# Optimization experiments

Measured on AMD Instinct MI355X. Metric: run time of the kernel, lower is better.

The kernel has to match this reference:

```python
import jax, jax.numpy as jnp
import numpy as np

# ----- config (matches init_kwargs) -----
DATA_SIZE = 128
WIDTH = 512
DEPTH = 3          # hidden layers in eqx.nn.MLP
NUM_BLOCKS = 2
BATCH = 512
NSTEPS = 10        # (t1 - t0) / dt0 = 1.0 / 0.1
T1 = 1.0
DT = -0.1          # integrate t1 -> t0

# Tsit5 Butcher tableau (5th-order solution weights; b7 = 0 so stage 7 is skipped)
TS_C = [0.0, 0.161, 0.327, 0.9, 0.9800255409045097, 1.0]
TS_A = [
    [],
    [0.161],
    [-0.008480655492356989, 0.335480655492357],
    [2.8971530571054935, -6.359448489975075, 4.3622954328695815],
    [5.325864828439257, -11.748883564062828, 7.4955393428898365, -0.09249506636175525],
    [5.86145544294642, -12.92096931784711, 8.159367898576159, -0.071584973281401, -0.028269050394068383],
]
TS_B = [0.09646076681806523, 0.01, 0.4798896504144996, 1.379008574103742, -3.290069515436081, 2.324710524099774]


def setup_inputs() -> dict:
    key = jax.random.key(0)
    ks = jax.random.split(key, 10)
    d, w, nb = DATA_SIZE, WIDTH, NUM_BLOCKS
    in0 = d + 1  # autonomous=False: t is concatenated to y

    def init(k, shape, fan_in):
        return jax.random.normal(k, shape, dtype=jnp.float32) / np.sqrt(fan_in).astype(np.float32)

    return {
        "y": jax.random.normal(ks[0], (BATCH, d), dtype=jnp.float32),
        "Ws0": init(ks[1], (nb, in0, w), in0), "bs0": init(ks[2], (nb, w), w),
        "Ws1": init(ks[3], (nb, w, w), w),     "bs1": init(ks[4], (nb, w), w),
        "Ws2": init(ks[5], (nb, w, w), w),     "bs2": init(ks[6], (nb, w), w),
        "Ws3": init(ks[7], (nb, w, d), w),     "bs3": init(ks[8], (nb, d), d),
    }


def _mlp(inp, layers):
    # inp: [in_size] vector (per-sample), relu hidden activations, linear output
    h = inp
    for W, b in layers[:-1]:
        h = jax.nn.relu(h @ W + b)
    W, b = layers[-1]
    return h @ W + b


def _field_and_trace(t, y, layers):
    # y: [B, d]. Exact log-det trace via vmapped vjp over identity (exact_logp_wrapper).
    eye = jnp.eye(DATA_SIZE, dtype=y.dtype)

    def single(yy):
        fn = lambda z: _mlp(jnp.concatenate([jnp.full((1,), t, yy.dtype), z]), layers)
        f, vjp_fn = jax.vjp(fn, yy)
        (dfdy,) = jax.vmap(vjp_fn)(eye)  # [d, d] Jacobian
        return f, jnp.trace(dfdy)

    return jax.vmap(single)(y)


def _solve_block(y, lp, layers):
    # Fixed-step Tsit5 on augmented state (y, logp), t1 -> t0, 10 steps.
    def step(carry, n):
        y, lp = carry
        t = jnp.float32(T1) + jnp.float32(DT) * n.astype(jnp.float32)
        ky, klp = [], []
        for i in range(6):
            ti = t + jnp.float32(TS_C[i] * DT)
            yi = y
            for j in range(i):
                yi = yi + jnp.float32(DT * TS_A[i][j]) * ky[j]
            fy, flp = _field_and_trace(ti, yi, layers)
            ky.append(fy)
            klp.append(flp)
        for i in range(6):
            y = y + jnp.float32(DT * TS_B[i]) * ky[i]
            lp = lp + jnp.float32(DT * TS_B[i]) * klp[i]
        return (y, lp), None

    (y, lp), _ = jax.lax.scan(step, (y, lp), jnp.arange(NSTEPS))
    return y, lp


def reference(y, Ws0, bs0, Ws1, bs1, Ws2, bs2, Ws3, bs3):
    lp = jnp.zeros((y.shape[0],), dtype=y.dtype)  # delta log-likelihood
    for b in range(NUM_BLOCKS):
        layers = [(Ws0[b], bs0[b]), (Ws1[b], bs1[b]), (Ws2[b], bs2[b]), (Ws3[b], bs3[b])]
        y, lp = _solve_block(y, lp, layers)
    # normal_log_likelihood (faithful to source: log(2*pi) NOT scaled by d)
    log2pi = np.float32(np.log(2.0 * np.pi))
    return lp + (-0.5) * (log2pi + jnp.sum(y * y, axis=-1))
```

## Files before the change

kernel.cpp:

```cpp
#include <hip/hip_runtime.h>


using short8 = __attribute__((ext_vector_type(8))) short;
using u16x8  = __attribute__((ext_vector_type(8))) unsigned short;
using f32x4v = __attribute__((ext_vector_type(4))) float;
using i32x4  = __attribute__((ext_vector_type(4))) int;
using u32x4  = __attribute__((ext_vector_type(4))) unsigned;
using i32x16 = __attribute__((ext_vector_type(16))) int;

__device__ __forceinline__ unsigned short f2bf(float f) {
  union { float f; unsigned u; } v; v.f = f;
  unsigned r = v.u + 0x7fffu + ((v.u >> 16) & 1u);
  return (unsigned short)(r >> 16);
}
__device__ __forceinline__ float bf2f(unsigned short h) {
  union { unsigned u; float f; } v; v.u = ((unsigned)h) << 16; return v.f;
}
__device__ __forceinline__ signed char q8(float v, float inv) {
  float r = rintf(v * inv);
  r = fminf(fmaxf(r, -127.f), 127.f);
  return (signed char)(int)r;
}

typedef const __attribute__((address_space(1))) void gas_t;
typedef __attribute__((address_space(3))) void las_t;
__device__ __forceinline__ void gl_lds16(const void* g, void* l) {
  __builtin_amdgcn_global_load_lds((gas_t*)g, (las_t*)l, 16, 0, 0);
}

struct Coef6 { float v[6]; };

#define INV_S0 254.0f
#define INV_S1 508.0f
#define SCALE_J 7.7500155e-06f
#define SCALE_G 3.8750077e-06f

__global__ __launch_bounds__(256) void init_state(const float* __restrict__ y_in,
                                                  float* __restrict__ y,
                                                  float* __restrict__ lp) {
  int i = blockIdx.x * 256 + threadIdx.x;
  if (i < 512 * 128) y[i] = y_in[i];
  if (i < 512) lp[i] = 0.f;
}

__global__ __launch_bounds__(256) void cast_weights(
    const float* __restrict__ W0, const float* __restrict__ W1,
    const float* __restrict__ W2, const float* __restrict__ W3,
    signed char* __restrict__ w0q,
    unsigned short* __restrict__ w0tH, unsigned short* __restrict__ w0tL,
    unsigned short* __restrict__ w1tH, unsigned short* __restrict__ w1tL,
    signed char* __restrict__ w1q,
    unsigned short* __restrict__ w2tH, unsigned short* __restrict__ w2tL,
    unsigned short* __restrict__ w3tH, unsigned short* __restrict__ w3tL,
    signed char* __restrict__ w3q, signed char* __restrict__ w2q) {
  int i = blockIdx.x * 256 + threadIdx.x;
  if (i < 65536) {
    int j = i >> 9, a = i & 511;
    w0q[i] = q8(W0[(1 + j) * 512 + a], INV_S0);
    return;
  }
  i -= 65536;
  if (i >= 2 * 65536 + 2 * 262144) {
    int q = i - (2 * 65536 + 2 * 262144);
    if (q < 262144) w2q[q] = q8(W2[q], INV_S1);
    return;
  }
  float v;
  unsigned short* dh;
  unsigned short* dl;
  signed char* qd = nullptr;
  int di;
  if (i < 65536) {
    int n = i >> 7, k = i & 127;
    v = W0[(1 + k) * 512 + n]; dh = w0tH; dl = w0tL; di = i;
  } else if (i < 65536 + 262144) {
    int q = i - 65536; int n = q >> 9, k = q & 511;
    v = W1[k * 512 + n]; dh = w1tH; dl = w1tL; di = q; qd = w1q;
  } else if (i < 65536 + 2 * 262144) {
    int q = i - 65536 - 262144; int c = q >> 9, b = q & 511;
    v = W2[b * 512 + c]; dh = w2tH; dl = w2tL; di = q;
  } else {
    int q = i - 65536 - 2 * 262144; int j = q >> 9, c = q & 511;
    v = W3[c * 128 + j]; dh = w3tH; dl = w3tL; di = q; qd = w3q;
  }
  unsigned short hi = f2bf(v);
  dh[di] = hi;
  dl[di] = f2bf(v - bf2f(hi));
  if (qd) qd[di] = q8(v, INV_S1);
}

template <bool RELU>
__global__ __launch_bounds__(256, 2) void fwd_mfma(
    const unsigned short* __restrict__ Ahi, const unsigned short* __restrict__ Alo,
    const unsigned short* __restrict__ WtH, const unsigned short* __restrict__ WtL,
    const float* __restrict__ bias,
    float* __restrict__ Cf, unsigned short* __restrict__ Hhi,
    unsigned short* __restrict__ Hlo, int N, int K) {
  __shared__ unsigned short AsH[2][4096], AsL[2][4096], BsH[2][4096], BsL[2][4096];
  const int t = threadIdx.x, l = t & 63, w = t >> 6;
  const int wm = w >> 1, wn = w & 1, lr = l & 15, lg = l >> 4;
  const int m0 = blockIdx.y * 32, n0 = blockIdx.x * 32;
  const int lr7 = lr & 7;

  auto stage = [&](int cur, int k0) {
#pragma unroll
    for (int r = 0; r < 2; ++r) {
      int g = r * 256 + t;
      int row = g >> 4, gc = g & 15;
      size_t co = (size_t)k0 + ((gc ^ (row & 7)) << 3);
      size_t ao = (size_t)(m0 + row) * K + co;
      size_t bo = (size_t)(n0 + row) * K + co;
      int db = (r * 256 + (t & 192)) * 16;
      gl_lds16(Ahi + ao, (char*)AsH[cur] + db);
      gl_lds16(Alo + ao, (char*)AsL[cur] + db);
      gl_lds16(WtH + bo, (char*)BsH[cur] + db);
      gl_lds16(WtL + bo, (char*)BsL[cur] + db);
    }
  };

  f32x4v acc = {0.f, 0.f, 0.f, 0.f};
  stage(0, 0);
  __syncthreads();
  int cur = 0;
  for (int k0 = 0; k0 < K; k0 += 128) {
    if (k0 + 128 < K) stage(cur ^ 1, k0 + 128);
#pragma unroll
    for (int ks = 0; ks < 4; ++ks) {
      int sl = ((ks * 4 + lg) ^ lr7) << 4;
      int ab = (wm * 16 + lr) * 256 + sl;
      int bb = (wn * 16 + lr) * 256 + sl;
      short8 ah = *(const short8*)((const char*)AsH[cur] + ab);
      short8 al = *(const short8*)((const char*)AsL[cur] + ab);
      short8 bh = *(const short8*)((const char*)BsH[cur] + bb);
      short8 bl = *(const short8*)((const char*)BsL[cur] + bb);
      acc = __builtin_amdgcn_mfma_f32_16x16x32_bf16(ah, bh, acc, 0, 0, 0);
      acc = __builtin_amdgcn_mfma_f32_16x16x32_bf16(ah, bl, acc, 0, 0, 0);
      acc = __builtin_amdgcn_mfma_f32_16x16x32_bf16(al, bh, acc, 0, 0, 0);
    }
    __syncthreads();
    cur ^= 1;
  }

  int n = n0 + wn * 16 + lr;
  float be = bias[n];
#pragma unroll
  for (int r = 0; r < 4; ++r) {
    int m = m0 + wm * 16 + lg * 4 + r;
    float v = acc[r] + be;
    if (RELU) {
      v = fmaxf(v, 0.f);
      unsigned short h = f2bf(v);
      Hhi[m * N + n] = h;
      Hlo[m * N + n] = f2bf(v - bf2f(h));
    } else {
      Cf[m * N + n] = v;
    }
  }
}

__global__ __launch_bounds__(256, 2) void jac_l0(
    int l0n,
    const signed char* __restrict__ w1q, const signed char* __restrict__ w0q,
    const signed char* __restrict__ w2q, const signed char* __restrict__ w3q,
    const unsigned short* __restrict__ d0m, const unsigned short* __restrict__ d1m,
    const unsigned short* __restrict__ d2m, float* __restrict__ klp,
    const float* __restrict__ yb, const float* __restrict__ kyb, Coef6 ca, int nc,
    const unsigned short* __restrict__ WtH, const unsigned short* __restrict__ WtL,
    const float* __restrict__ bias, const float* __restrict__ wrow0, float tval,
    unsigned short* __restrict__ Hhi, unsigned short* __restrict__ Hlo) {
  __shared__ __align__(16) char smraw[68672];
  const int t = threadIdx.x, l = t & 63, w = t >> 6;

  if ((int)blockIdx.x < l0n) {
    unsigned short* AsH = (unsigned short*)(smraw);
    unsigned short* AsL = (unsigned short*)(smraw + 8192);
    unsigned short* BsH = (unsigned short*)(smraw + 16384);
    unsigned short* BsL = (unsigned short*)(smraw + 24576);
    const int lb = blockIdx.x;
    const int wm = w >> 1, wn = w & 1, lr = l & 15, lg = l >> 4, lr7 = lr & 7;
    const int m0 = (lb >> 4) * 32, n0 = (lb & 15) * 32;

#pragma unroll
    for (int r = 0; r < 2; ++r) {
      int g = r * 256 + t;
      int row = g >> 4;
      int gc = (g & 15) ^ (row & 7);
      size_t bo = (size_t)(n0 + row) * 128 + gc * 8;
      int db = (r * 256 + (t & 192)) * 16;
      gl_lds16(WtH + bo, (char*)BsH + db);
      gl_lds16(WtL + bo, (char*)BsL + db);
    }
    {
      int row = t >> 3, seg = t & 7;
      int gidx = (m0 + row) * 128 + seg * 16;
      float x[16];
#pragma unroll
      for (int q = 0; q < 4; ++q)
        *(float4*)&x[q * 4] = *(const float4*)&yb[gidx + q * 4];
      for (int j2 = 0; j2 < nc; ++j2) {
        float c = ca.v[j2];
#pragma unroll
        for (int q = 0; q < 4; ++q) {
          float4 u = *(const float4*)&kyb[j2 * 65536 + gidx + q * 4];
          x[q * 4 + 0] = fmaf(c, u.x, x[q * 4 + 0]);
          x[q * 4 + 1] = fmaf(c, u.y, x[q * 4 + 1]);
          x[q * 4 + 2] = fmaf(c, u.z, x[q * 4 + 2]);
          x[q * 4 + 3] = fmaf(c, u.w, x[q * 4 + 3]);
        }
      }
      u16x8 h8[2], l8[2];
#pragma unroll
      for (int e = 0; e < 16; ++e) {
        unsigned short hh = f2bf(x[e]);
        h8[e >> 3][e & 7] = hh;
        l8[e >> 3][e & 7] = f2bf(x[e] - bf2f(hh));
      }
#pragma unroll
      for (int h = 0; h < 2; ++h) {
        int gx = (seg * 2 + h) ^ (row & 7);
        *(u16x8*)((char*)AsH + row * 256 + gx * 16) = h8[h];
        *(u16x8*)((char*)AsL + row * 256 + gx * 16) = l8[h];
      }
    }
    __syncthreads();

    f32x4v acc = {0.f, 0.f, 0.f, 0.f};
#pragma unroll
    for (int ks = 0; ks < 4; ++ks) {
      int sl = ((ks * 4 + lg) ^ lr7) << 4;
      int ab = (wm * 16 + lr) * 256 + sl;
      int bb = (wn * 16 + lr) * 256 + sl;
      short8 ah = *(const short8*)((const char*)AsH + ab);
      short8 al = *(const short8*)((const char*)AsL + ab);
      short8 bh = *(const short8*)((const char*)BsH + bb);
      short8 bl = *(const short8*)((const char*)BsL + bb);
      acc = __builtin_amdgcn_mfma_f32_16x16x32_bf16(ah, bh, acc, 0, 0, 0);
      acc = __builtin_amdgcn_mfma_f32_16x16x32_bf16(ah, bl, acc, 0, 0, 0);
      acc = __builtin_amdgcn_mfma_f32_16x16x32_bf16(al, bh, acc, 0, 0, 0);
    }

    int n = n0 + wn * 16 + lr;
    float be = fmaf(tval, wrow0[n], bias[n]);
#pragma unroll
    for (int r = 0; r < 4; ++r) {
      int m = m0 + wm * 16 + lg * 4 + r;
      float v = fmaxf(acc[r] + be, 0.f);
      unsigned short h = f2bf(v);
      Hhi[m * 512 + n] = h;
      Hlo[m * 512 + n] = f2bf(v - bf2f(h));
    }
    return;
  }

  signed char* As = (signed char*)smraw;
  signed char* Bs = (signed char*)(smraw + 32768);
  unsigned char* Ms8 = (unsigned char*)(smraw + 65536);
  float* red = (float*)(smraw + 68608);
  const int jx = blockIdx.x - l0n;
  const int cb = jx & 3, s0 = (jx >> 2) * 2;
  const int wm = w >> 1, wn = w & 1;
  const int lr31 = l & 31, hi = l >> 5;

  if (w < 3) {
    const unsigned short* src = (w == 0) ? d0m : (w == 1) ? d1m : d2m;
    gl_lds16(src + (size_t)s0 * 512 + l * 8, As + w * 2048);
    gl_lds16(src + (size_t)(s0 + 1) * 512 + l * 8, As + w * 2048 + 1024);
  }
  __syncthreads();
  {
    const unsigned* Mraw = (const unsigned*)As;
    unsigned* Mout = (unsigned*)Ms8;
#pragma unroll
    for (int q = 0; q < 3; ++q) {
      int i = q * 256 + t;
      unsigned lo = Mraw[2 * i], hi2 = Mraw[2 * i + 1];
      unsigned m = 0;
      if (lo & 0xFFFFu) m |= 0x000000FFu;
      if (lo >> 16)     m |= 0x0000FF00u;
      if (hi2 & 0xFFFFu) m |= 0x00FF0000u;
      if (hi2 >> 16)     m |= 0xFF000000u;
      Mout[i] = m;
    }
  }
  __syncthreads();

  auto stage = [&](int buf, const signed char* Aq, const signed char* Bq, int k0) {
#pragma unroll
    for (int i = 0; i < 8; ++i) {
      int u = i * 4 + w;
      int uu = (u < 16) ? u : (u - 16);
      int g = uu * 64 + l;
      int row = g & 127;
      int kh = (g >> 7) & 1;
      int ks = g >> 8;
      int kb = k0 + ks * 32 + kh * 16;
      if (u < 16)
        gl_lds16(Aq + (size_t)(cb * 128 + row) * 512 + kb, As + buf * 16384 + uu * 1024);
      else
        gl_lds16(Bq + (size_t)row * 512 + kb, Bs + buf * 16384 + uu * 1024);
    }
  };

  i32x16 a0[2][2], a1[2][2];
  auto phase = [&](const signed char* Aq, const signed char* Bq, int mbase) {
#pragma unroll
    for (int mt = 0; mt < 2; ++mt)
#pragma unroll
      for (int nt = 0; nt < 2; ++nt) {
        a0[mt][nt] = (i32x16)(0);
        a1[mt][nt] = (i32x16)(0);
      }
    stage(0, Aq, Bq, 0);
    int cur = 0;
    for (int k0 = 0; k0 < 512; k0 += 128) {
      if (k0 + 128 < 512) {
        stage(cur ^ 1, Aq, Bq, k0 + 128);
        asm volatile("s_waitcnt vmcnt(8)" ::: "memory");
      } else {
        asm volatile("s_waitcnt vmcnt(0)" ::: "memory");
      }
      asm volatile("s_barrier" ::: "memory");
      __builtin_amdgcn_s_setprio(1);
#pragma unroll
      for (int ks = 0; ks < 4; ++ks) {
        i32x4 af[2];
#pragma unroll
        for (int mt = 0; mt < 2; ++mt)
          af[mt] = *(const i32x4*)(As + cur * 16384 +
                                   (ks * 256 + hi * 128 + wm * 64 + mt * 32 + lr31) * 16);
        u32x4 mk0 = *(const u32x4*)&Ms8[mbase + k0 + ks * 32 + hi * 16];
        u32x4 mk1 = *(const u32x4*)&Ms8[mbase + 512 + k0 + ks * 32 + hi * 16];
#pragma unroll
        for (int nt = 0; nt < 2; ++nt) {
          u32x4 bv = *(const u32x4*)(Bs + cur * 16384 +
                                     (ks * 256 + hi * 128 + wn * 64 + nt * 32 + lr31) * 16);
          i32x4 b0 = (i32x4)(bv & mk0);
          i32x4 b1 = (i32x4)(bv & mk1);
#pragma unroll
          for (int mt = 0; mt < 2; ++mt) {
            a0[mt][nt] = __builtin_amdgcn_mfma_i32_32x32x32_i8(af[mt], b0,
                                                               a0[mt][nt], 0, 0, 0);
            a1[mt][nt] = __builtin_amdgcn_mfma_i32_32x32x32_i8(af[mt], b1,
                                                               a1[mt][nt], 0, 0, 0);
          }
        }
      }
      __builtin_amdgcn_s_setprio(0);
      asm volatile("s_waitcnt lgkmcnt(0)" ::: "memory");
      asm volatile("s_barrier" ::: "memory");
      cur ^= 1;
    }
  };

  phase(w2q, w3q, 2 * 1024);
  unsigned pg0[2][2][8], pg1[2][2][8];
#pragma unroll
  for (int mt = 0; mt < 2; ++mt)
#pragma unroll
    for (int nt = 0; nt < 2; ++nt)
#pragma unroll
      for (int p = 0; p < 8; ++p) {
        float ga = (float)a0[mt][nt][2 * p] * SCALE_G;
        float gb = (float)a0[mt][nt][2 * p + 1] * SCALE_G;
        float gc = (float)a1[mt][nt][2 * p] * SCALE_G;
        float gd = (float)a1[mt][nt][2 * p + 1] * SCALE_G;
        asm("v_cvt_pk_bf16_f32 %0, %1, %2" : "=v"(pg0[mt][nt][p]) : "v"(ga), "v"(gb));
        asm("v_cvt_pk_bf16_f32 %0, %1, %2" : "=v"(pg1[mt][nt][p]) : "v"(gc), "v"(gd));
      }

  phase(w1q, w0q, 0);

  float p0 = 0.f, p1 = 0.f;
  const unsigned char* D1b = &Ms8[1 * 1024];
#pragma unroll
  for (int mt = 0; mt < 2; ++mt) {
#pragma unroll
    for (int q = 0; q < 4; ++q) {
      int blg = cb * 128 + wm * 64 + mt * 32 + q * 8 + 4 * hi;
      uchar4 m40 = *(const uchar4*)&D1b[blg];
      uchar4 m41 = *(const uchar4*)&D1b[512 + blg];
      unsigned char mm0[4] = {m40.x, m40.y, m40.z, m40.w};
      unsigned char mm1[4] = {m41.x, m41.y, m41.z, m41.w};
#pragma unroll
      for (int e = 0; e < 4; ++e) {
        const int r = q * 4 + e;
#pragma unroll
        for (int nt = 0; nt < 2; ++nt) {
          unsigned pw0 = pg0[mt][nt][r >> 1];
          unsigned pw1 = pg1[mt][nt][r >> 1];
          unsigned short g0 = (r & 1) ? (unsigned short)(pw0 >> 16)
                                      : (unsigned short)(pw0 & 0xFFFFu);
          unsigned short g1 = (r & 1) ? (unsigned short)(pw1 >> 16)
                                      : (unsigned short)(pw1 & 0xFFFFu);
          if (mm0[e]) p0 = fmaf((float)a0[mt][nt][r], bf2f(g0), p0);
          if (mm1[e]) p1 = fmaf((float)a1[mt][nt][r], bf2f(g1), p1);
        }
      }
    }
  }
  p0 *= SCALE_J;
  p1 *= SCALE_J;
#pragma unroll
  for (int off = 1; off < 64; off <<= 1) {
    p0 += __shfl_xor(p0, off);
    p1 += __shfl_xor(p1, off);
  }
  if (l == 0) { red[w * 2] = p0; red[w * 2 + 1] = p1; }
  __syncthreads();
  if (t < 2) {
    klp[cb * 512 + s0 + t] = red[t] + red[2 + t] + red[4 + t] + red[6 + t];
  }
}

__global__ __launch_bounds__(256) void step_update(float* __restrict__ y,
                                                   float* __restrict__ lp,
                                                   const float* __restrict__ ky,
                                                   const float* __restrict__ klp_part,
                                                   Coef6 db) {
  int i = blockIdx.x * 256 + threadIdx.x;
  if (i < 65536) {
    float a = y[i];
#pragma unroll
    for (int j = 0; j < 6; ++j) a += db.v[j] * ky[j * 65536 + i];
    y[i] = a;
  }
  if (i < 512) {
    float l = lp[i];
#pragma unroll
    for (int j = 0; j < 6; ++j) {
      const float* kp = klp_part + j * 2048;
      float tr = kp[i] + kp[512 + i] + kp[1024 + i] + kp[1536 + i];
      l += db.v[j] * tr;
    }
    lp[i] = l;
  }
}

__global__ __launch_bounds__(64) void finalize(const float* __restrict__ y,
                                               const float* __restrict__ lp,
                                               float* __restrict__ out) {
  int s = blockIdx.x, l = threadIdx.x;
  float v0 = y[s * 128 + l], v1 = y[s * 128 + 64 + l];
  float sum = v0 * v0 + v1 * v1;
#pragma unroll
  for (int off = 32; off; off >>= 1) sum += __shfl_down(sum, off);
  if (l == 0) out[s] = lp[s] + (-0.5f) * (1.8378770664093453f + sum);
}

extern "C" void kernel_launch(void* const* d_in, const int* in_sizes, int n_in,
                              void* d_out, int out_size, void* d_ws, size_t ws_size,
                              hipStream_t stream) {
  const float* y_in = (const float*)d_in[0];
  const float* Ws0 = (const float*)d_in[1];
  const float* bs0 = (const float*)d_in[2];
  const float* Ws1 = (const float*)d_in[3];
  const float* bs1 = (const float*)d_in[4];
  const float* Ws2 = (const float*)d_in[5];
  const float* bs2 = (const float*)d_in[6];
  const float* Ws3 = (const float*)d_in[7];
  const float* bs3 = (const float*)d_in[8];
  float* out = (float*)d_out;

  char* ws = (char*)d_ws;
  size_t off = 0;
  auto alloc = [&](size_t bytes) {
    void* p = ws + off;
    off = (off + bytes + 255) & ~(size_t)255;
    return p;
  };
  float* y  = (float*)alloc(65536 * 4);
  float* lp = (float*)alloc(512 * 4);
  unsigned short* h0hi[2] = {(unsigned short*)alloc(262144 * 2),
                             (unsigned short*)alloc(262144 * 2)};
  unsigned short* h0lo[2] = {(unsigned short*)alloc(262144 * 2),
                             (unsigned short*)alloc(262144 * 2)};
  unsigned short* h1hi = (unsigned short*)alloc(262144 * 2);
  unsigned short* h1lo = (unsigned short*)alloc(262144 * 2);
  unsigned short* h2hi = (unsigned short*)alloc(262144 * 2);
  unsigned short* h2lo = (unsigned short*)alloc(262144 * 2);
  float* ky  = (float*)alloc(6 * 65536 * 4);
  float* klp = (float*)alloc(6 * 2048 * 4);
  unsigned short* w0tH = (unsigned short*)alloc(65536 * 2);
  unsigned short* w0tL = (unsigned short*)alloc(65536 * 2);
  unsigned short* w1tH = (unsigned short*)alloc(262144 * 2);
  unsigned short* w1tL = (unsigned short*)alloc(262144 * 2);
  unsigned short* w2tH = (unsigned short*)alloc(262144 * 2);
  unsigned short* w2tL = (unsigned short*)alloc(262144 * 2);
  unsigned short* w3tH = (unsigned short*)alloc(65536 * 2);
  unsigned short* w3tL = (unsigned short*)alloc(65536 * 2);
  signed char* w0q = (signed char*)alloc(65536);
  signed char* w1q = (signed char*)alloc(262144);
  signed char* w2q = (signed char*)alloc(262144);
  signed char* w3q = (signed char*)alloc(65536);
  (void)ws_size; (void)in_sizes; (void)n_in; (void)out_size;

  static const double DT = -0.1;
  static const double TC[6] = {0.0, 0.161, 0.327, 0.9, 0.9800255409045097, 1.0};
  static const double TA[6][5] = {
      {0, 0, 0, 0, 0},
      {0.161, 0, 0, 0, 0},
      {-0.008480655492356989, 0.335480655492357, 0, 0, 0},
      {2.8971530571054935, -6.359448489975075, 4.3622954328695815, 0, 0},
      {5.325864828439257, -11.748883564062828, 7.4955393428898365, -0.09249506636175525, 0},
      {5.86145544294642, -12.92096931784711, 8.159367898576159, -0.071584973281401,
       -0.028269050394068383}};
  static const double TB[6] = {0.09646076681806523, 0.01, 0.4798896504144996,
                               1.379008574103742, -3.290069515436081, 2.324710524099774};

  Coef6 db;
  for (int i2 = 0; i2 < 6; ++i2) db.v[i2] = (float)(DT * TB[i2]);

  init_state<<<dim3(256), dim3(256), 0, stream>>>(y_in, y, lp);

  for (int blk = 0; blk < 2; ++blk) {
    const float* W0 = Ws0 + blk * 129 * 512;
    const float* b0 = bs0 + blk * 512;
    const float* W1 = Ws1 + blk * 262144;
    const float* b1 = bs1 + blk * 512;
    const float* W2 = Ws2 + blk * 262144;
    const float* b2 = bs2 + blk * 512;
    const float* W3 = Ws3 + blk * 65536;
    const float* b3 = bs3 + blk * 128;

    cast_weights<<<dim3(3840), dim3(256), 0, stream>>>(
        W0, W1, W2, W3, w0q, w0tH, w0tL, w1tH, w1tL, w1q,
        w2tH, w2tL, w3tH, w3tL, w3q, w2q);

    for (int n = 0; n < 10; ++n) {
      float tn = 1.0f + (-0.1f) * (float)n;
      for (int i = 0; i < 6; ++i) {
        const int p = i & 1;
        if (n == 0 && i == 0) {
          Coef6 c0 = {{0, 0, 0, 0, 0, 0}};
          jac_l0<<<dim3(256), 256, 0, stream>>>(
              256, w1q, w0q, w2q, w3q, h0hi[0], h1hi, h2hi, klp,
              y, ky, c0, 0, w0tH, w0tL, b0, W0, tn, h0hi[0], h0lo[0]);
        }
        fwd_mfma<true><<<dim3(16, 16), 256, 0, stream>>>(
            h0hi[p], h0lo[p], w1tH, w1tL, b1, nullptr, h1hi, h1lo, 512, 512);
        fwd_mfma<true><<<dim3(16, 16), 256, 0, stream>>>(
            h1hi, h1lo, w2tH, w2tL, b2, nullptr, h2hi, h2lo, 512, 512);
        fwd_mfma<false><<<dim3(4, 16), 256, 0, stream>>>(
            h2hi, h2lo, w3tH, w3tL, b3, ky + i * 65536, nullptr, nullptr, 128, 512);

        if (i < 5) {
          Coef6 cn = {{0, 0, 0, 0, 0, 0}};
          for (int j = 0; j <= i; ++j) cn.v[j] = (float)(DT * TA[i + 1][j]);
          float tin = tn + (float)(TC[i + 1] * DT);
          jac_l0<<<dim3(1280), 256, 0, stream>>>(
              256, w1q, w0q, w2q, w3q, h0hi[p], h1hi, h2hi, klp + i * 2048,
              y, ky, cn, i + 1, w0tH, w0tL, b0, W0, tin, h0hi[p ^ 1], h0lo[p ^ 1]);
        } else if (n < 9) {
          float tin = tn - 0.1f;
          jac_l0<<<dim3(1280), 256, 0, stream>>>(
              256, w1q, w0q, w2q, w3q, h0hi[p], h1hi, h2hi, klp + 5 * 2048,
              y, ky, db, 6, w0tH, w0tL, b0, W0, tin, h0hi[p ^ 1], h0lo[p ^ 1]);
        } else {
          Coef6 c0 = {{0, 0, 0, 0, 0, 0}};
          jac_l0<<<dim3(1024), 256, 0, stream>>>(
              0, w1q, w0q, w2q, w3q, h0hi[p], h1hi, h2hi, klp + 5 * 2048,
              y, ky, c0, 0, w0tH, w0tL, b0, W0, tn, h0hi[p ^ 1], h0lo[p ^ 1]);
        }
      }
      step_update<<<dim3(256), dim3(256), 0, stream>>>(y, lp, ky, klp, db);
    }
  }
  finalize<<<dim3(512), dim3(64), 0, stream>>>(y, lp, out);
}
```

Before: 7.379 ms.

## Fuse output-layer GEMM into Jacobian/next-stage kernel with atomic gate

Removes the separate fwd_mfma launch for the final 512->128 layer and folds it into the combined Jacobian/layer-0 kernel as 64 extra leading blocks. The layer-0 blocks of the next stage now spin on a global atomic counter until all 64 output blocks have written ky, then read the newest ky with atomic loads. This saves one kernel launch per stage and lets the Jacobian blocks overlap with the output GEMM. The cost is inter-block spin-waiting, which depends on the lower-index blocks being scheduled first to avoid deadlock, plus a per-stage gate counter.

```diff
diff --git a/kernel.cpp b/kernel.cpp
--- a/kernel.cpp
+++ b/kernel.cpp
@@ -37,10 +37,12 @@
 
 __global__ __launch_bounds__(256) void init_state(const float* __restrict__ y_in,
                                                   float* __restrict__ y,
-                                                  float* __restrict__ lp) {
+                                                  float* __restrict__ lp,
+                                                  int* __restrict__ gates) {
   int i = blockIdx.x * 256 + threadIdx.x;
   if (i < 512 * 128) y[i] = y_in[i];
   if (i < 512) lp[i] = 0.f;
+  if (i < 128) gates[i] = 0;
 }
 
 __global__ __launch_bounds__(256) void cast_weights(
@@ -158,25 +160,91 @@
   }
 }
 
-__global__ __launch_bounds__(256, 2) void jac_l0(
-    int l0n,
+__global__ __launch_bounds__(256, 2) void mega(
+    int l3n, int jacn, int l0n, int gated, int* __restrict__ gate,
+    const unsigned short* __restrict__ h2hi, const unsigned short* __restrict__ h2lo,
+    const unsigned short* __restrict__ w3tH, const unsigned short* __restrict__ w3tL,
+    const float* __restrict__ b3, float* __restrict__ kyout,
     const signed char* __restrict__ w1q, const signed char* __restrict__ w0q,
     const signed char* __restrict__ w2q, const signed char* __restrict__ w3q,
     const unsigned short* __restrict__ d0m, const unsigned short* __restrict__ d1m,
-    const unsigned short* __restrict__ d2m, float* __restrict__ klp,
+    float* __restrict__ klp,
     const float* __restrict__ yb, const float* __restrict__ kyb, Coef6 ca, int nc,
     const unsigned short* __restrict__ WtH, const unsigned short* __restrict__ WtL,
     const float* __restrict__ bias, const float* __restrict__ wrow0, float tval,
     unsigned short* __restrict__ Hhi, unsigned short* __restrict__ Hlo) {
   __shared__ __align__(16) char smraw[68672];
   const int t = threadIdx.x, l = t & 63, w = t >> 6;
-
-  if ((int)blockIdx.x < l0n) {
+  const int bx = blockIdx.x;
+
+  if (bx < l3n) {
+    unsigned short* AsH = (unsigned short*)(smraw);
+    unsigned short* AsL = (unsigned short*)(smraw + 16384);
+    unsigned short* BsH = (unsigned short*)(smraw + 32768);
+    unsigned short* BsL = (unsigned short*)(smraw + 49152);
+    const int wm = w >> 1, wn = w & 1, lr = l & 15, lg = l >> 4, lr7 = lr & 7;
+    const int m0 = (bx >> 2) * 32, n0 = (bx & 3) * 32;
+    const int K = 512, N = 128;
+
+    auto stage = [&](int cur, int k0) {
+#pragma unroll
+      for (int r = 0; r < 2; ++r) {
+        int g = r * 256 + t;
+        int row = g >> 4, gc = g & 15;
+        size_t co = (size_t)k0 + ((gc ^ (row & 7)) << 3);
+        size_t ao = (size_t)(m0 + row) * K + co;
+        size_t bo = (size_t)(n0 + row) * K + co;
+        int db = (r * 256 + (t & 192)) * 16 + cur * 8192;
+        gl_lds16(h2hi + ao, (char*)AsH + db);
+        gl_lds16(h2lo + ao, (char*)AsL + db);
+        gl_lds16(w3tH + bo, (char*)BsH + db);
+        gl_lds16(w3tL + bo, (char*)BsL + db);
+      }
+    };
+
+    f32x4v acc = {0.f, 0.f, 0.f, 0.f};
+    stage(0, 0);
+    __syncthreads();
+    int cur = 0;
+    for (int k0 = 0; k0 < K; k0 += 128) {
+      if (k0 + 128 < K) stage(cur ^ 1, k0 + 128);
+#pragma unroll
+      for (int ks = 0; ks < 4; ++ks) {
+        int sl = ((ks * 4 + lg) ^ lr7) << 4;
+        int ab = (wm * 16 + lr) * 256 + sl + cur * 8192;
+        int bb = (wn * 16 + lr) * 256 + sl + cur * 8192;
+        short8 ah = *(const short8*)((const char*)AsH + ab);
+        short8 al = *(const short8*)((const char*)AsL + ab);
+        short8 bh = *(const short8*)((const char*)BsH + bb);
+        short8 bl = *(const short8*)((const char*)BsL + bb);
+        acc = __builtin_amdgcn_mfma_f32_16x16x32_bf16(ah, bh, acc, 0, 0, 0);
+        acc = __builtin_amdgcn_mfma_f32_16x16x32_bf16(ah, bl, acc, 0, 0, 0);
+        acc = __builtin_amdgcn_mfma_f32_16x16x32_bf16(al, bh, acc, 0, 0, 0);
+      }
+      __syncthreads();
+      cur ^= 1;
+    }
+
+    int n = n0 + wn * 16 + lr;
+    float be = b3[n];
+#pragma unroll
+    for (int r = 0; r < 4; ++r) {
+      int m = m0 + wm * 16 + lg * 4 + r;
+      __hip_atomic_store(&kyout[m * N + n], acc[r] + be, __ATOMIC_RELAXED,
+                         __HIP_MEMORY_SCOPE_AGENT);
+    }
+    __threadfence();
+    __syncthreads();
+    if (t == 0) atomicAdd(gate, 1);
+    return;
+  }
+
+  if (bx >= l3n + jacn) {
     unsigned short* AsH = (unsigned short*)(smraw);
     unsigned short* AsL = (unsigned short*)(smraw + 8192);
     unsigned short* BsH = (unsigned short*)(smraw + 16384);
     unsigned short* BsL = (unsigned short*)(smraw + 24576);
-    const int lb = blockIdx.x;
+    const int lb = bx - l3n - jacn;
     const int wm = w >> 1, wn = w & 1, lr = l & 15, lg = l >> 4, lr7 = lr & 7;
     const int m0 = (lb >> 4) * 32, n0 = (lb & 15) * 32;
 
@@ -190,6 +258,15 @@
       gl_lds16(WtH + bo, (char*)BsH + db);
       gl_lds16(WtL + bo, (char*)BsL + db);
     }
+    if (gated) {
+      if (t == 0) {
+        while (__hip_atomic_load(gate, __ATOMIC_ACQUIRE,
+                                 __HIP_MEMORY_SCOPE_AGENT) < 64) {
+          __builtin_amdgcn_s_sleep(8);
+        }
+      }
+      __syncthreads();
+    }
     {
       int row = t >> 3, seg = t & 7;
       int gidx = (m0 + row) * 128 + seg * 16;
@@ -199,13 +276,22 @@
         *(float4*)&x[q * 4] = *(const float4*)&yb[gidx + q * 4];
       for (int j2 = 0; j2 < nc; ++j2) {
         float c = ca.v[j2];
-#pragma unroll
-        for (int q = 0; q < 4; ++q) {
-          float4 u = *(const float4*)&kyb[j2 * 65536 + gidx + q * 4];
-          x[q * 4 + 0] = fmaf(c, u.x, x[q * 4 + 0]);
-          x[q * 4 + 1] = fmaf(c, u.y, x[q * 4 + 1]);
-          x[q * 4 + 2] = fmaf(c, u.z, x[q * 4 + 2]);
-          x[q * 4 + 3] = fmaf(c, u.w, x[q * 4 + 3]);
+        if (gated && j2 == nc - 1) {
+#pragma unroll
+          for (int e = 0; e < 16; ++e) {
+            float u = __hip_atomic_load((float*)&kyb[j2 * 65536 + gidx + e],
+                                        __ATOMIC_RELAXED, __HIP_MEMORY_SCOPE_AGENT);
+            x[e] = fmaf(c, u, x[e]);
+          }
+        } else {
+#pragma unroll
+          for (int q = 0; q < 4; ++q) {
+            float4 u = *(const float4*)&kyb[j2 * 65536 + gidx + q * 4];
+            x[q * 4 + 0] = fmaf(c, u.x, x[q * 4 + 0]);
+            x[q * 4 + 1] = fmaf(c, u.y, x[q * 4 + 1]);
+            x[q * 4 + 2] = fmaf(c, u.z, x[q * 4 + 2]);
+            x[q * 4 + 3] = fmaf(c, u.w, x[q * 4 + 3]);
+          }
         }
       }
       u16x8 h8[2], l8[2];
@@ -256,13 +342,13 @@
   signed char* Bs = (signed char*)(smraw + 32768);
   unsigned char* Ms8 = (unsigned char*)(smraw + 65536);
   float* red = (float*)(smraw + 68608);
-  const int jx = blockIdx.x - l0n;
+  const int jx = bx - l3n;
   const int cb = jx & 3, s0 = (jx >> 2) * 2;
   const int wm = w >> 1, wn = w & 1;
   const int lr31 = l & 31, hi = l >> 5;
 
   if (w < 3) {
-    const unsigned short* src = (w == 0) ? d0m : (w == 1) ? d1m : d2m;
+    const unsigned short* src = (w == 0) ? d0m : (w == 1) ? d1m : h2hi;
     gl_lds16(src + (size_t)s0 * 512 + l * 8, As + w * 2048);
     gl_lds16(src + (size_t)(s0 + 1) * 512 + l * 8, As + w * 2048 + 1024);
   }
@@ -470,6 +556,7 @@
   };
   float* y  = (float*)alloc(65536 * 4);
   float* lp = (float*)alloc(512 * 4);
+  int* gates = (int*)alloc(128 * 4);
   unsigned short* h0hi[2] = {(unsigned short*)alloc(262144 * 2),
                              (unsigned short*)alloc(262144 * 2)};
   unsigned short* h0lo[2] = {(unsigned short*)alloc(262144 * 2),
@@ -509,8 +596,9 @@
 
   Coef6 db;
   for (int i2 = 0; i2 < 6; ++i2) db.v[i2] = (float)(DT * TB[i2]);
-
-  init_state<<<dim3(256), dim3(256), 0, stream>>>(y_in, y, lp);
+  Coef6 c0 = {{0, 0, 0, 0, 0, 0}};
+
+  init_state<<<dim3(256), dim3(256), 0, stream>>>(y_in, y, lp, gates);
 
   for (int blk = 0; blk < 2; ++blk) {
     const float* W0 = Ws0 + blk * 129 * 512;
@@ -530,35 +618,36 @@
       float tn = 1.0f + (-0.1f) * (float)n;
       for (int i = 0; i < 6; ++i) {
         const int p = i & 1;
+        const int gid = blk * 60 + n * 6 + i;
         if (n == 0 && i == 0) {
-          Coef6 c0 = {{0, 0, 0, 0, 0, 0}};
-          jac_l0<<<dim3(256), 256, 0, stream>>>(
-              256, w1q, w0q, w2q, w3q, h0hi[0], h1hi, h2hi, klp,
+          mega<<<dim3(256), 256, 0, stream>>>(
+              0, 0, 256, 0, gates, h2hi, h2lo, w3tH, w3tL, b3, ky,
+              w1q, w0q, w2q, w3q, h0hi[0], h1hi, klp,
               y, ky, c0, 0, w0tH, w0tL, b0, W0, tn, h0hi[0], h0lo[0]);
         }
         fwd_mfma<true><<<dim3(16, 16), 256, 0, stream>>>(
             h0hi[p], h0lo[p], w1tH, w1tL, b1, nullptr, h1hi, h1lo, 512, 512);
         fwd_mfma<true><<<dim3(16, 16), 256, 0, stream>>>(
             h1hi, h1lo, w2tH, w2tL, b2, nullptr, h2hi, h2lo, 512, 512);
-        fwd_mfma<false><<<dim3(4, 16), 256, 0, stream>>>(
-            h2hi, h2lo, w3tH, w3tL, b3, ky + i * 65536, nullptr, nullptr, 128, 512);
 
         if (i < 5) {
           Coef6 cn = {{0, 0, 0, 0, 0, 0}};
           for (int j = 0; j <= i; ++j) cn.v[j] = (float)(DT * TA[i + 1][j]);
           float tin = tn + (float)(TC[i + 1] * DT);
-          jac_l0<<<dim3(1280), 256, 0, stream>>>(
-              256, w1q, w0q, w2q, w3q, h0hi[p], h1hi, h2hi, klp + i * 2048,
+          mega<<<dim3(1344), 256, 0, stream>>>(
+              64, 1024, 256, 1, gates + gid, h2hi, h2lo, w3tH, w3tL, b3,
+              ky + i * 65536, w1q, w0q, w2q, w3q, h0hi[p], h1hi, klp + i * 2048,
               y, ky, cn, i + 1, w0tH, w0tL, b0, W0, tin, h0hi[p ^ 1], h0lo[p ^ 1]);
         } else if (n < 9) {
           float tin = tn - 0.1f;
-          jac_l0<<<dim3(1280), 256, 0, stream>>>(
-              256, w1q, w0q, w2q, w3q, h0hi[p], h1hi, h2hi, klp + 5 * 2048,
+          mega<<<dim3(1344), 256, 0, stream>>>(
+              64, 1024, 256, 1, gates + gid, h2hi, h2lo, w3tH, w3tL, b3,
+              ky + 5 * 65536, w1q, w0q, w2q, w3q, h0hi[p], h1hi, klp + 5 * 2048,
               y, ky, db, 6, w0tH, w0tL, b0, W0, tin, h0hi[p ^ 1], h0lo[p ^ 1]);
         } else {
-          Coef6 c0 = {{0, 0, 0, 0, 0, 0}};
-          jac_l0<<<dim3(1024), 256, 0, stream>>>(
-              0, w1q, w0q, w2q, w3q, h0hi[p], h1hi, h2hi, klp + 5 * 2048,
+          mega<<<dim3(1088), 256, 0, stream>>>(
+              64, 1024, 0, 0, gates + gid, h2hi, h2lo, w3tH, w3tL, b3,
+              ky + 5 * 65536, w1q, w0q, w2q, w3q, h0hi[p], h1hi, klp + 5 * 2048,
               y, ky, c0, 0, w0tH, w0tL, b0, W0, tn, h0hi[p ^ 1], h0lo[p ^ 1]);
         }
       }
```

Result: no change. 7.483 ms (+1.4%).
